# Kernel optimization log

Hardware: AMD Instinct MI355X
Metric: run time of the kernel (lower is better)

The kernel has to match this reference:

```python
import jax, jax.numpy as jnp
import numpy as np

B, N, C = 4, 2048, 768
H, QK_R, VP_R = 12, 32, 32  # heads, per-head q/k rank, per-head v rank
HEAD_DIM = 64               # original head_dim -> scale = head_dim ** -0.5


def setup_inputs() -> dict:
    key = jax.random.key(0)
    kx, kq, kk, kv, kp = jax.random.split(key, 5)
    s = lambda fan_in: 1.0 / np.sqrt(fan_in)
    return {
        "x": jax.random.normal(kx, (B, N, C), dtype=jnp.float32),
        "Wq": jax.random.normal(kq, (C, H * QK_R), dtype=jnp.float32) * s(C),
        "Wk": jax.random.normal(kk, (C, H * QK_R), dtype=jnp.float32) * s(C),
        "Wv": jax.random.normal(kv, (C, H * VP_R), dtype=jnp.float32) * s(C),
        "Wp": jax.random.normal(kp, (H * VP_R, C), dtype=jnp.float32) * s(H * VP_R),
    }


def reference(x, Wq, Wk, Wv, Wp):
    b, n, c = x.shape
    scale = HEAD_DIM ** -0.5
    # low-rank projections, split per head: [B, H, N, r]
    q = (x @ Wq).reshape(b, n, H, QK_R).transpose(0, 2, 1, 3)
    k = (x @ Wk).reshape(b, n, H, QK_R).transpose(0, 2, 1, 3)
    v = (x @ Wv).reshape(b, n, H, VP_R).transpose(0, 2, 1, 3)
    attn = jnp.einsum("bhnr,bhmr->bhnm", q, k) * scale  # [B, H, N, N]
    attn = jax.nn.softmax(attn, axis=-1)                 # attn_drop rate 0 -> identity
    out = jnp.einsum("bhnm,bhmr->bhnr", attn, v)        # [B, H, N, VP_R]
    out = out.transpose(0, 2, 1, 3).reshape(b, n, H * VP_R)
    return out @ Wp                                      # proj_drop rate 0 -> identity
```

## Files before the change

### kernel.cpp

```cpp
#include <hip/hip_runtime.h>
#include <hip/hip_bf16.h>
#include <stdint.h>
#include <math.h>

#define B_   4
#define N_   2048
#define C_   768
#define H_   12
#define R_   32
#define M_   (B_ * N_)
#define QKV_ (H_ * R_)

#define QSCALE 0.18033688011112042f

#define KST 40
#define VST 136

typedef __attribute__((ext_vector_type(8))) short    bf16x8;
typedef __attribute__((ext_vector_type(4))) float    f32x4;
typedef __attribute__((ext_vector_type(8))) unsigned short u16x8;
typedef __attribute__((ext_vector_type(4))) _Float16 f16x4;
typedef __attribute__((ext_vector_type(8))) _Float16 f16x8;

#if defined(__has_builtin)
#if __has_builtin(__builtin_amdgcn_exp2f)
#define EXP2F(x) __builtin_amdgcn_exp2f(x)
#else
#define EXP2F(x) exp2f(x)
#endif
#else
#define EXP2F(x) exp2f(x)
#endif

__device__ __forceinline__ short f2bf(float f) {
    union { float f; uint32_t u; } v; v.f = f;
    uint32_t u = v.u;
    uint32_t r = (u + 0x7fffu + ((u >> 16) & 1u)) >> 16;
    return (short)r;
}

__device__ __forceinline__ uint32_t packbf2(float a, float b) {
    __hip_bfloat162 h = __float22bfloat162_rn(float2{a, b});
    uint32_t u; __builtin_memcpy(&u, &h, 4); return u;
}

__device__ __forceinline__ uint32_t packh2(float a, float b) {
    auto h = __builtin_amdgcn_cvt_pkrtz(a, b);
    uint32_t u; __builtin_memcpy(&u, &h, 4); return u;
}

__device__ __forceinline__ void gll16(const short* g, short* l) {
    __builtin_amdgcn_global_load_lds(
        (const __attribute__((address_space(1))) uint32_t*)g,
        (__attribute__((address_space(3))) uint32_t*)l, 16, 0, 0);
}

__global__ __launch_bounds__(256) void prep(
    const float* __restrict__ X,
    const float* __restrict__ Wq, const float* __restrict__ Wk,
    const float* __restrict__ Wv, const float* __restrict__ Wp,
    short* __restrict__ wts, short* __restrict__ wpt, short* __restrict__ Xb) {
    int bid = blockIdx.x;
    if (bid < 288) {
        __shared__ short Ls[64 * 65];
        int z = bid / 72;
        int t = bid - z * 72;
        const float* src; float scl; short* dst; int trt, tct, Psrc, Pdst;
        if (z < 3) {
            trt = t / 6; tct = t - (t / 6) * 6;
            Psrc = 384; Pdst = 768;
            src = (z == 0) ? Wq : (z == 1) ? Wk : Wv;
            scl = (z == 0) ? QSCALE : 1.0f;
            dst = wts + (size_t)z * (QKV_ * C_);
        } else {
            trt = t / 12; tct = t - (t / 12) * 12;
            Psrc = 768; Pdst = 384;
            src = Wp; scl = 1.0f; dst = wpt;
        }
        int r0 = trt * 64, c0 = tct * 64;
        int rr = threadIdx.x >> 2;
        int cc = (threadIdx.x & 3) * 16;
        const float4* s4 = (const float4*)(src + (size_t)(r0 + rr) * Psrc + c0 + cc);
        float4 f0 = s4[0], f1 = s4[1], f2 = s4[2], f3 = s4[3];
        short* lp = &Ls[rr * 65 + cc];
        lp[0]=f2bf(f0.x*scl); lp[1]=f2bf(f0.y*scl); lp[2]=f2bf(f0.z*scl); lp[3]=f2bf(f0.w*scl);
        lp[4]=f2bf(f1.x*scl); lp[5]=f2bf(f1.y*scl); lp[6]=f2bf(f1.z*scl); lp[7]=f2bf(f1.w*scl);
        lp[8]=f2bf(f2.x*scl); lp[9]=f2bf(f2.y*scl); lp[10]=f2bf(f2.z*scl); lp[11]=f2bf(f2.w*scl);
        lp[12]=f2bf(f3.x*scl); lp[13]=f2bf(f3.y*scl); lp[14]=f2bf(f3.z*scl); lp[15]=f2bf(f3.w*scl);
        __syncthreads();
        int jr = threadIdx.x >> 2;
        int seg = (threadIdx.x & 3) * 16;
        u16x8 o0, o1;
        #pragma unroll
        for (int u = 0; u < 8; u++) {
            o0[u] = (unsigned short)Ls[(seg + u) * 65 + jr];
            o1[u] = (unsigned short)Ls[(seg + 8 + u) * 65 + jr];
        }
        short* dp = dst + (size_t)(c0 + jr) * Pdst + r0 + seg;
        *(u16x8*)dp = o0;
        *(u16x8*)(dp + 8) = o1;
    } else {
        size_t i = ((size_t)(bid - 288) * 256 + threadIdx.x) * 8;
        const float4* s4 = (const float4*)(X + i);
        float4 f0 = s4[0], f1 = s4[1];
        u16x8 o;
        o[0]=f2bf(f0.x); o[1]=f2bf(f0.y); o[2]=f2bf(f0.z); o[3]=f2bf(f0.w);
        o[4]=f2bf(f1.x); o[5]=f2bf(f1.y); o[6]=f2bf(f1.z); o[7]=f2bf(f1.w);
        *(u16x8*)(Xb + i) = o;
    }
}

__global__ __launch_bounds__(256, 4) void qkv_gemm(
    const short* __restrict__ Xb, const short* __restrict__ wts,
    short* __restrict__ qkvout) {
    const int mt = blockIdx.x, nt = blockIdx.y;
    const int m0 = mt * 128, j0 = nt * 64;
    const int z = nt / 6;

    __shared__ short smem[128 * 64 + 64 * 64];
    short* As = smem;
    short* Bs = smem + 128 * 64;
    short* Tt = smem;

    const int tid = threadIdx.x;
    const int lane = tid & 63, w = tid >> 6;
    const int l16 = lane & 15, quad = lane >> 4;

    const int sarow = w * 32 + (lane >> 3);
    const int sbrow = w * 16 + (lane >> 3);
    const int scol = (((lane & 7) ^ (lane >> 3))) * 8;
    const short* pa = Xb  + (size_t)(m0 + sarow) * C_ + scol;
    const short* pb = wts + (size_t)(j0 + sbrow) * C_ + scol;

    f32x4 acc[2][4] = {};

    for (int k0 = 0; k0 < C_; k0 += 64) {
        __syncthreads();
        #pragma unroll
        for (int j = 0; j < 4; j++)
            gll16(pa + (size_t)j * 8 * C_ + k0, &As[(w * 32 + j * 8) * 64]);
        #pragma unroll
        for (int j = 0; j < 2; j++)
            gll16(pb + (size_t)j * 8 * C_ + k0, &Bs[(w * 16 + j * 8) * 64]);
        __syncthreads();
        #pragma unroll
        for (int ks = 0; ks < 2; ks++) {
            bf16x8 af[2], bf[4];
            #pragma unroll
            for (int i = 0; i < 2; i++) {
                int ar = w * 32 + i * 16 + l16;
                af[i] = *(const bf16x8*)&As[ar * 64 + (((ks * 4 + quad) ^ (ar & 7)) * 8)];
            }
            #pragma unroll
            for (int c = 0; c < 4; c++) {
                int br = c * 16 + l16;
                bf[c] = *(const bf16x8*)&Bs[br * 64 + (((ks * 4 + quad) ^ (br & 7)) * 8)];
            }
            #pragma unroll
            for (int i = 0; i < 2; i++)
                #pragma unroll
                for (int c = 0; c < 4; c++)
                    acc[i][c] = __builtin_amdgcn_mfma_f32_16x16x32_bf16(af[i], bf[c], acc[i][c], 0, 0, 0);
        }
    }

    const size_t S = (size_t)B_ * H_ * N_ * R_;
    if (z < 2) {
        short* outz = qkvout + (size_t)z * S;
        #pragma unroll
        for (int c = 0; c < 4; c++) {
            int jz = (nt - z * 6) * 64 + c * 16 + l16;
            int h = jz >> 5, r = jz & 31;
            #pragma unroll
            for (int i = 0; i < 2; i++) {
                #pragma unroll
                for (int reg = 0; reg < 4; reg++) {
                    int m = m0 + w * 32 + i * 16 + quad * 4 + reg;
                    int bb = m >> 11, n = m & (N_ - 1);
                    outz[(((size_t)(bb * H_ + h)) * N_ + n) * R_ + r] = f2bf(acc[i][c][reg]);
                }
            }
        }
    } else {
        const int bb = m0 >> 11;
        const int nl0 = m0 & (N_ - 1);
        short* vout = qkvout + 2 * S;
        __syncthreads();
        #pragma unroll
        for (int i = 0; i < 2; i++)
            #pragma unroll
            for (int c = 0; c < 4; c++) {
                uint32_t d0 = packh2(acc[i][c][0], acc[i][c][1]);
                uint32_t d1 = packh2(acc[i][c][2], acc[i][c][3]);
                uint2 dd = {d0, d1};
                *(uint2*)&Tt[(c * 16 + l16) * 132 + w * 32 + i * 16 + quad * 4] = dd;
            }
        __syncthreads();
        int jr = tid >> 2;
        int seg = (tid & 3) * 32;
        int jz = (nt - 12) * 64 + jr;
        int hh = jz >> 5, rr = jz & 31;
        short* dst = vout + (((size_t)(bb * H_ + hh)) * R_ + rr) * N_ + nl0 + seg;
        #pragma unroll
        for (int q4 = 0; q4 < 4; q4++) {
            u16x8 vv = *(const u16x8*)&Tt[jr * 132 + seg + q4 * 8];
            *(u16x8*)(dst + q4 * 8) = vv;
        }
    }
}

__global__ __launch_bounds__(512, 6) void attn(
    const short* __restrict__ qkv, short* __restrict__ O) {
    const int qt = blockIdx.x, h = blockIdx.y, b = blockIdx.z;
    const size_t S = (size_t)B_ * H_ * N_ * R_;
    const short* Q  = qkv + ((size_t)(b * H_ + h)) * N_ * R_;
    const short* K  = qkv + S + ((size_t)(b * H_ + h)) * N_ * R_;
    const short* Vt = qkv + 2 * S + ((size_t)(b * H_ + h)) * R_ * N_;

    __shared__ short sbuf[2 * 128 * KST + 2 * 32 * VST];
    short* Ksb = sbuf;
    short* Vsb = sbuf + 2 * 128 * KST;

    const int tid = threadIdx.x;
    const int lane = tid & 63, wave = tid >> 6;
    const int wq = wave & 3, wk = wave >> 2;
    const int l16 = lane & 15, quad = lane >> 4;

    bf16x8 aq[2];
    #pragma unroll
    for (int g = 0; g < 2; g++)
        aq[g] = *(const bf16x8*)(Q + (size_t)(qt * 128 + wq * 32 + g * 16 + l16) * R_ + quad * 8);

    f16x8 ones8;
    #pragma unroll
    for (int j = 0; j < 8; j++) ones8[j] = (_Float16)1.0f;

    f32x4 o0T[2] = {}, o1T[2] = {}, lacc[2] = {};

    const int krow = tid >> 2;
    const int kseg = (tid & 3) * 8;
    const short* kgp = K + (size_t)krow * R_ + kseg;
    const int kwoff = krow * KST + kseg;
    const int vrow = tid >> 4;
    const int vcol = (tid & 15) * 8;
    const short* vgp = Vt + (size_t)vrow * N_ + vcol;
    const int vwoff = vrow * VST + vcol;

    {
        u16x8 ka = *(const u16x8*)kgp;
        u16x8 va = *(const u16x8*)vgp;
        *(u16x8*)&Ksb[kwoff] = ka;
        *(u16x8*)&Vsb[vwoff] = va;
    }
    __syncthreads();

    for (int it = 0; it < 16; ++it) {
        const int kt0 = it * 128;
        const int cur = it & 1;
        u16x8 kn, vn;
        if (it < 15) {
            kn = *(const u16x8*)(kgp + (size_t)(kt0 + 128) * R_);
            vn = *(const u16x8*)(vgp + kt0 + 128);
        }

        const short* Kc = &Ksb[cur * 128 * KST];
        const short* Vc = &Vsb[cur * 32 * VST];

        bf16x8 kf[4];
        #pragma unroll
        for (int c = 0; c < 4; c++)
            kf[c] = *(const bf16x8*)&Kc[((wk * 4 + c) * 16 + l16) * KST + quad * 8];

        #pragma unroll
        for (int p = 0; p < 2; p++) {
            const int pp = wk * 2 + p;
            union V8 { struct { f16x4 lo, hi; } h; f16x8 v; };
            V8 v0u, v1u;
            v0u.h.lo = *(const f16x4*)&Vc[l16 * VST + pp * 32 + quad * 4];
            v0u.h.hi = *(const f16x4*)&Vc[l16 * VST + pp * 32 + 16 + quad * 4];
            v1u.h.lo = *(const f16x4*)&Vc[(16 + l16) * VST + pp * 32 + quad * 4];
            v1u.h.hi = *(const f16x4*)&Vc[(16 + l16) * VST + pp * 32 + 16 + quad * 4];
            #pragma unroll
            for (int g = 0; g < 2; g++) {
                f32x4 zz = {};
                f32x4 s0 = __builtin_amdgcn_mfma_f32_16x16x32_bf16(kf[2 * p],     aq[g], zz, 0, 0, 0);
                f32x4 s1 = __builtin_amdgcn_mfma_f32_16x16x32_bf16(kf[2 * p + 1], aq[g], zz, 0, 0, 0);
                union { f16x8 v; uint32_t w[4]; } pu;
                pu.w[0] = packh2(EXP2F(s0[0]), EXP2F(s0[1]));
                pu.w[1] = packh2(EXP2F(s0[2]), EXP2F(s0[3]));
                pu.w[2] = packh2(EXP2F(s1[0]), EXP2F(s1[1]));
                pu.w[3] = packh2(EXP2F(s1[2]), EXP2F(s1[3]));
                o0T[g]  = __builtin_amdgcn_mfma_f32_16x16x32_f16(v0u.v, pu.v, o0T[g], 0, 0, 0);
                o1T[g]  = __builtin_amdgcn_mfma_f32_16x16x32_f16(v1u.v, pu.v, o1T[g], 0, 0, 0);
                lacc[g] = __builtin_amdgcn_mfma_f32_16x16x32_f16(ones8, pu.v, lacc[g], 0, 0, 0);
            }
        }

        if (it < 15) {
            *(u16x8*)&Ksb[(cur ^ 1) * 128 * KST + kwoff] = kn;
            *(u16x8*)&Vsb[(cur ^ 1) * 32 * VST + vwoff]  = vn;
        }
        __syncthreads();
    }

    float* sm = (float*)sbuf;
    if (wk == 1) {
        #pragma unroll
        for (int g = 0; g < 2; g++) {
            int id = (wq * 2 + g) * 64 + lane;
            *(f32x4*)&sm[id * 4]        = o0T[g];
            *(f32x4*)&sm[2048 + id * 4] = o1T[g];
            sm[4096 + id] = lacc[g][0];
        }
    }
    __syncthreads();
    if (wk == 0) {
        #pragma unroll
        for (int g = 0; g < 2; g++) {
            int id = (wq * 2 + g) * 64 + lane;
            f32x4 p0 = *(const f32x4*)&sm[id * 4];
            f32x4 p1 = *(const f32x4*)&sm[2048 + id * 4];
            float pl = sm[4096 + id];
            f32x4 a0 = o0T[g] + p0;
            f32x4 a1 = o1T[g] + p1;
            float inv = 1.0f / (lacc[g][0] + pl);
            int n = qt * 128 + wq * 32 + g * 16 + l16;
            size_t base = ((size_t)b * N_ + n) * QKV_ + h * R_;
            uint32_t a0w = packbf2(a0[0] * inv, a0[1] * inv);
            uint32_t a1w = packbf2(a0[2] * inv, a0[3] * inv);
            uint2 s0 = {a0w, a1w};
            *(uint2*)&O[base + quad * 4] = s0;
            uint32_t b0w = packbf2(a1[0] * inv, a1[1] * inv);
            uint32_t b1w = packbf2(a1[2] * inv, a1[3] * inv);
            uint2 s1 = {b0w, b1w};
            *(uint2*)&O[base + 16 + quad * 4] = s1;
        }
    }
}

__global__ __launch_bounds__(256, 3) void out_gemm(
    const short* __restrict__ Ob, const short* __restrict__ wpt,
    float* __restrict__ out) {
    const int mt = blockIdx.x, nt = blockIdx.y;
    const int m0 = mt * 128, j0 = nt * 64;

    __shared__ short As[128 * 64];
    __shared__ short Bs[64 * 64];

    const int tid = threadIdx.x;
    const int lane = tid & 63, w = tid >> 6;
    const int l16 = lane & 15, quad = lane >> 4;

    const int sarow = w * 32 + (lane >> 3);
    const int sbrow = w * 16 + (lane >> 3);
    const int scol = (((lane & 7) ^ (lane >> 3))) * 8;
    const short* pa = Ob  + (size_t)(m0 + sarow) * QKV_ + scol;
    const short* pb = wpt + (size_t)(j0 + sbrow) * QKV_ + scol;

    f32x4 acc[2][4] = {};

    for (int k0 = 0; k0 < QKV_; k0 += 64) {
        __syncthreads();
        #pragma unroll
        for (int j = 0; j < 4; j++)
            gll16(pa + (size_t)j * 8 * QKV_ + k0, &As[(w * 32 + j * 8) * 64]);
        #pragma unroll
        for (int j = 0; j < 2; j++)
            gll16(pb + (size_t)j * 8 * QKV_ + k0, &Bs[(w * 16 + j * 8) * 64]);
        __syncthreads();
        #pragma unroll
        for (int ks = 0; ks < 2; ks++) {
            bf16x8 af[2], bf[4];
            #pragma unroll
            for (int i = 0; i < 2; i++) {
                int ar = w * 32 + i * 16 + l16;
                af[i] = *(const bf16x8*)&As[ar * 64 + (((ks * 4 + quad) ^ (ar & 7)) * 8)];
            }
            #pragma unroll
            for (int c = 0; c < 4; c++) {
                int br = c * 16 + l16;
                bf[c] = *(const bf16x8*)&Bs[br * 64 + (((ks * 4 + quad) ^ (br & 7)) * 8)];
            }
            #pragma unroll
            for (int i = 0; i < 2; i++)
                #pragma unroll
                for (int c = 0; c < 4; c++)
                    acc[i][c] = __builtin_amdgcn_mfma_f32_16x16x32_bf16(af[i], bf[c], acc[i][c], 0, 0, 0);
        }
    }

    #pragma unroll
    for (int i = 0; i < 2; i++)
        #pragma unroll
        for (int c = 0; c < 4; c++)
            #pragma unroll
            for (int reg = 0; reg < 4; reg++) {
                int m = m0 + w * 32 + i * 16 + quad * 4 + reg;
                out[(size_t)m * C_ + j0 + c * 16 + l16] = acc[i][c][reg];
            }
}

extern "C" void kernel_launch(void* const* d_in, const int* in_sizes, int n_in,
                              void* d_out, int out_size, void* d_ws, size_t ws_size,
                              hipStream_t stream) {
    const float* x  = (const float*)d_in[0];
    const float* Wq = (const float*)d_in[1];
    const float* Wk = (const float*)d_in[2];
    const float* Wv = (const float*)d_in[3];
    const float* Wp = (const float*)d_in[4];
    float* out = (float*)d_out;

    short* ws16 = (short*)d_ws;
    short* wts  = ws16;
    short* wpt  = wts + (size_t)3 * QKV_ * C_;
    short* qkv  = wpt + (size_t)QKV_ * C_;
    short* Obuf = qkv + (size_t)3 * B_ * H_ * N_ * R_;
    short* Xb   = Obuf + (size_t)B_ * N_ * QKV_;

    prep<<<dim3(288 + 3072), 256, 0, stream>>>(x, Wq, Wk, Wv, Wp, wts, wpt, Xb);
    qkv_gemm<<<dim3(M_ / 128, 18), 256, 0, stream>>>(Xb, wts, qkv);
    attn<<<dim3(N_ / 128, H_, B_), 512, 0, stream>>>(qkv, Obuf);
    out_gemm<<<dim3(M_ / 128, C_ / 64), 256, 0, stream>>>(Obuf, wpt, out);
}
```

Measured before the change: 153.6 us.

## Widen QKV GEMM tile to 128x96 and remap attention blocks per XCD

The QKV projection GEMM moves from 128x64 to 128x96 output tiles with a 2x2 wave layout, each wave holding 4x3 MFMA accumulators. This gives more MFMA work per LDS fragment load and cuts the grid from 18 to 12 column tiles. The V-transpose epilogue is rewritten to fit the wider tile. Separately, the attention launch becomes a 1D grid whose block index is remapped so that all query tiles of a (batch, head) land on the same XCD, aiming at better L2 reuse of K/V. The larger accumulator set raises register pressure and may lower occupancy.

```diff
diff --git a/kernel.cpp b/kernel.cpp
--- a/kernel.cpp
+++ b/kernel.cpp
@@ -114,10 +114,10 @@
     const short* __restrict__ Xb, const short* __restrict__ wts,
     short* __restrict__ qkvout) {
     const int mt = blockIdx.x, nt = blockIdx.y;
-    const int m0 = mt * 128, j0 = nt * 64;
-    const int z = nt / 6;
-
-    __shared__ short smem[128 * 64 + 64 * 64];
+    const int m0 = mt * 128, j0 = nt * 96;
+    const int z = nt >> 2;
+
+    __shared__ short smem[128 * 64 + 96 * 64];
     short* As = smem;
     short* Bs = smem + 128 * 64;
     short* Tt = smem;
@@ -125,14 +125,15 @@
     const int tid = threadIdx.x;
     const int lane = tid & 63, w = tid >> 6;
     const int l16 = lane & 15, quad = lane >> 4;
+    const int wm = w & 1, wn = w >> 1;
 
     const int sarow = w * 32 + (lane >> 3);
-    const int sbrow = w * 16 + (lane >> 3);
+    const int sbrow = w * 24 + (lane >> 3);
     const int scol = (((lane & 7) ^ (lane >> 3))) * 8;
     const short* pa = Xb  + (size_t)(m0 + sarow) * C_ + scol;
     const short* pb = wts + (size_t)(j0 + sbrow) * C_ + scol;
 
-    f32x4 acc[2][4] = {};
+    f32x4 acc[4][3] = {};
 
     for (int k0 = 0; k0 < C_; k0 += 64) {
         __syncthreads();
@@ -140,26 +141,26 @@
         for (int j = 0; j < 4; j++)
             gll16(pa + (size_t)j * 8 * C_ + k0, &As[(w * 32 + j * 8) * 64]);
         #pragma unroll
-        for (int j = 0; j < 2; j++)
-            gll16(pb + (size_t)j * 8 * C_ + k0, &Bs[(w * 16 + j * 8) * 64]);
+        for (int j = 0; j < 3; j++)
+            gll16(pb + (size_t)j * 8 * C_ + k0, &Bs[(w * 24 + j * 8) * 64]);
         __syncthreads();
         #pragma unroll
         for (int ks = 0; ks < 2; ks++) {
-            bf16x8 af[2], bf[4];
-            #pragma unroll
-            for (int i = 0; i < 2; i++) {
-                int ar = w * 32 + i * 16 + l16;
+            bf16x8 af[4], bf[3];
+            #pragma unroll
+            for (int i = 0; i < 4; i++) {
+                int ar = wm * 64 + i * 16 + l16;
                 af[i] = *(const bf16x8*)&As[ar * 64 + (((ks * 4 + quad) ^ (ar & 7)) * 8)];
             }
             #pragma unroll
-            for (int c = 0; c < 4; c++) {
-                int br = c * 16 + l16;
+            for (int c = 0; c < 3; c++) {
+                int br = wn * 48 + c * 16 + l16;
                 bf[c] = *(const bf16x8*)&Bs[br * 64 + (((ks * 4 + quad) ^ (br & 7)) * 8)];
             }
             #pragma unroll
-            for (int i = 0; i < 2; i++)
+            for (int i = 0; i < 4; i++)
                 #pragma unroll
-                for (int c = 0; c < 4; c++)
+                for (int c = 0; c < 3; c++)
                     acc[i][c] = __builtin_amdgcn_mfma_f32_16x16x32_bf16(af[i], bf[c], acc[i][c], 0, 0, 0);
         }
     }
@@ -168,14 +169,14 @@
     if (z < 2) {
         short* outz = qkvout + (size_t)z * S;
         #pragma unroll
-        for (int c = 0; c < 4; c++) {
-            int jz = (nt - z * 6) * 64 + c * 16 + l16;
+        for (int c = 0; c < 3; c++) {
+            int jz = (nt & 3) * 96 + wn * 48 + c * 16 + l16;
             int h = jz >> 5, r = jz & 31;
             #pragma unroll
-            for (int i = 0; i < 2; i++) {
+            for (int i = 0; i < 4; i++) {
                 #pragma unroll
                 for (int reg = 0; reg < 4; reg++) {
-                    int m = m0 + w * 32 + i * 16 + quad * 4 + reg;
+                    int m = m0 + wm * 64 + i * 16 + quad * 4 + reg;
                     int bb = m >> 11, n = m & (N_ - 1);
                     outz[(((size_t)(bb * H_ + h)) * N_ + n) * R_ + r] = f2bf(acc[i][c][reg]);
                 }
@@ -187,31 +188,36 @@
         short* vout = qkvout + 2 * S;
         __syncthreads();
         #pragma unroll
-        for (int i = 0; i < 2; i++)
-            #pragma unroll
-            for (int c = 0; c < 4; c++) {
+        for (int i = 0; i < 4; i++)
+            #pragma unroll
+            for (int c = 0; c < 3; c++) {
                 uint32_t d0 = packh2(acc[i][c][0], acc[i][c][1]);
                 uint32_t d1 = packh2(acc[i][c][2], acc[i][c][3]);
                 uint2 dd = {d0, d1};
-                *(uint2*)&Tt[(c * 16 + l16) * 132 + w * 32 + i * 16 + quad * 4] = dd;
-            }
-        __syncthreads();
-        int jr = tid >> 2;
-        int seg = (tid & 3) * 32;
-        int jz = (nt - 12) * 64 + jr;
-        int hh = jz >> 5, rr = jz & 31;
-        short* dst = vout + (((size_t)(bb * H_ + hh)) * R_ + rr) * N_ + nl0 + seg;
-        #pragma unroll
-        for (int q4 = 0; q4 < 4; q4++) {
-            u16x8 vv = *(const u16x8*)&Tt[jr * 132 + seg + q4 * 8];
-            *(u16x8*)(dst + q4 * 8) = vv;
+                *(uint2*)&Tt[(wn * 48 + c * 16 + l16) * 136 + wm * 64 + i * 16 + quad * 4] = dd;
+            }
+        __syncthreads();
+        #pragma unroll
+        for (int u = 0; u < 6; u++) {
+            int ci = u * 256 + tid;
+            int jr = ci >> 4;
+            int c8 = (ci & 15) * 8;
+            int jz = (nt - 8) * 96 + jr;
+            int hh = jz >> 5, rr = jz & 31;
+            short* dst = vout + (((size_t)(bb * H_ + hh)) * R_ + rr) * N_ + nl0;
+            u16x8 vv = *(const u16x8*)&Tt[jr * 136 + c8];
+            *(u16x8*)(dst + c8) = vv;
         }
     }
 }
 
 __global__ __launch_bounds__(512, 6) void attn(
     const short* __restrict__ qkv, short* __restrict__ O) {
-    const int qt = blockIdx.x, h = blockIdx.y, b = blockIdx.z;
+    const int bid = blockIdx.x;
+    const int xcd = bid & 7, jj = bid >> 3;
+    const int bh = xcd * 6 + (jj >> 4);
+    const int qt = jj & 15;
+    const int b = bh / H_, h = bh - b * H_;
     const size_t S = (size_t)B_ * H_ * N_ * R_;
     const short* Q  = qkv + ((size_t)(b * H_ + h)) * N_ * R_;
     const short* K  = qkv + S + ((size_t)(b * H_ + h)) * N_ * R_;
@@ -418,7 +424,7 @@
     short* Xb   = Obuf + (size_t)B_ * N_ * QKV_;
 
     prep<<<dim3(288 + 3072), 256, 0, stream>>>(x, Wq, Wk, Wv, Wp, wts, wpt, Xb);
-    qkv_gemm<<<dim3(M_ / 128, 18), 256, 0, stream>>>(Xb, wts, qkv);
-    attn<<<dim3(N_ / 128, H_, B_), 512, 0, stream>>>(qkv, Obuf);
+    qkv_gemm<<<dim3(M_ / 128, 12), 256, 0, stream>>>(Xb, wts, qkv);
+    attn<<<dim3(768), 512, 0, stream>>>(qkv, Obuf);
     out_gemm<<<dim3(M_ / 128, C_ / 64), 256, 0, stream>>>(Obuf, wpt, out);
 }
```

Result: faster. 147.5 us (-3.9%).
